# Kernel tuning notes

Measured on AMD Instinct MI355X. Metric: run time of the kernel, lower is better.

## Reference

```python
import jax, jax.numpy as jnp
import numpy as np

N_NODES, N_EDGES, IN_F = 20000, 320000, 64
H1, H2 = 2, 2          # attn heads per GATv2 layer
D1, D2 = 128, 128      # gnn_size per layer
NM = [128, 128]        # nodemlp hidden sizes
EM = [512, 256]        # edgemlp hidden sizes
OUT_F = 1
NEG_SLOPE = 0.2


def _lin_init(key, fan_in, fan_out):
    kw, kb = jax.random.split(key)
    s = 1.0 / np.sqrt(fan_in)
    return (jax.random.uniform(kw, (fan_in, fan_out), jnp.float32, -s, s),
            jax.random.uniform(kb, (fan_out,), jnp.float32, -s, s))


def setup_inputs() -> dict:
    key = jax.random.key(0)
    ks = jax.random.split(key, 16)
    x = jax.random.normal(ks[0], (N_NODES, IN_F), jnp.float32)
    src = jax.random.randint(ks[1], (N_EDGES,), 0, N_NODES, jnp.int32)
    dst = jax.random.randint(ks[2], (N_EDGES,), 0, N_NODES, jnp.int32)
    # NodeMLP
    nw0, nb0 = _lin_init(ks[3], IN_F, NM[0])
    nw1, nb1 = _lin_init(ks[4], NM[0], NM[1])
    # GATv2 layer 1 (in=IN_F -> H1*D1)
    g1ws, g1bs = _lin_init(ks[5], IN_F, H1 * D1)
    g1wd, g1bd = _lin_init(ks[6], IN_F, H1 * D1)
    g1a = jax.random.normal(ks[7], (H1, D1), jnp.float32) * (1.0 / np.sqrt(D1))
    # GATv2 layer 2 (in=H1*D1 -> H2*D2)
    g2ws, g2bs = _lin_init(ks[8], H1 * D1, H2 * D2)
    g2wd, g2bd = _lin_init(ks[9], H1 * D1, H2 * D2)
    g2a = jax.random.normal(ks[10], (H2, D2), jnp.float32) * (1.0 / np.sqrt(D2))
    # EdgeMLP: in = 2*(NM[-1] + H2*D2) = 768
    e_in = 2 * (NM[-1] + H2 * D2)
    ew0, eb0 = _lin_init(ks[11], e_in, EM[0])
    ew1, eb1 = _lin_init(ks[12], EM[0], EM[1])
    ew2, eb2 = _lin_init(ks[13], EM[1], OUT_F)
    return dict(x=x, src=src, dst=dst,
                nw0=nw0, nb0=nb0, nw1=nw1, nb1=nb1,
                g1ws=g1ws, g1bs=g1bs, g1wd=g1wd, g1bd=g1bd, g1a=g1a,
                g2ws=g2ws, g2bs=g2bs, g2wd=g2wd, g2bd=g2bd, g2a=g2a,
                ew0=ew0, eb0=eb0, ew1=ew1, eb1=eb1, ew2=ew2, eb2=eb2)


def _segment_softmax(logits, dst, n):
    # logits: (E, H); softmax over edges sharing the same dst node
    m = jax.ops.segment_max(logits, dst, num_segments=n)
    e = jnp.exp(logits - m[dst])
    s = jax.ops.segment_sum(e, dst, num_segments=n)
    return e / s[dst]


def _gatv2(h, src, dst, ws, bs, wd, bd, attn, heads, dim, n):
    fs = (h @ ws + bs).reshape(n, heads, dim)   # fc_src
    fd = (h @ wd + bd).reshape(n, heads, dim)   # fc_dst
    e = jax.nn.leaky_relu(fs[src] + fd[dst], NEG_SLOPE)      # (E,H,D)
    logits = jnp.einsum('ehd,hd->eh', e, attn)               # (E,H)
    a = _segment_softmax(logits, dst, n)                      # (E,H)
    out = jax.ops.segment_sum(a[..., None] * fs[src], dst, num_segments=n)
    return jax.nn.relu(out).reshape(n, heads * dim)           # flatten heads


def reference(x, src, dst,
              nw0, nb0, nw1, nb1,
              g1ws, g1bs, g1wd, g1bd, g1a,
              g2ws, g2bs, g2wd, g2bd, g2a,
              ew0, eb0, ew1, eb1, ew2, eb2):
    n = x.shape[0]
    # NodeMLP (dropout=0 -> identity)
    h1 = jax.nn.relu(x @ nw0 + nb0)
    h1 = jax.nn.relu(h1 @ nw1 + nb1)
    # GCN: two GATv2Conv layers with relu activation, heads flattened
    h2 = _gatv2(x, src, dst, g1ws, g1bs, g1wd, g1bd, g1a, H1, D1, n)
    h2 = _gatv2(h2, src, dst, g2ws, g2bs, g2wd, g2bd, g2a, H2, D2, n)
    # EdgeMLP: gather src/dst, concat, MLP (relu before every layer but first)
    h = jnp.concatenate([h1[src], h1[dst], h2[src], h2[dst]], axis=1)  # (E,768)
    h = h @ ew0 + eb0
    h = jax.nn.relu(h) @ ew1 + eb1
    h = jax.nn.relu(h) @ ew2 + eb2
    return h  # (E, 1) edge scores
```

## Files before the change

kernel.cpp:

```cpp
#include <hip/hip_runtime.h>
#include <hip/hip_bf16.h>

constexpr int N_NODES = 20000;
constexpr int N_EDGES = 320000;

typedef _Float16 half8 __attribute__((ext_vector_type(8)));
typedef _Float16 half4 __attribute__((ext_vector_type(4)));
typedef float    f32x16 __attribute__((ext_vector_type(16)));

__device__ __forceinline__ float lrelu(float x) { return x > 0.f ? x : 0.2f * x; }

__global__ void scan_all_kernel(const int* __restrict__ counts,
                                int* __restrict__ row_off, int* __restrict__ cursor) {
    __shared__ int ps[1024];
    const int t = threadIdx.x;
    const int base = t * 20;
    int loc[20];
    int sum = 0;
#pragma unroll
    for (int i = 0; i < 20; ++i) {
        const int idx = base + i;
        const int v = (idx < N_NODES) ? counts[idx] : 0;
        loc[i] = sum;
        sum += v;
    }
    ps[t] = sum;
    __syncthreads();
    for (int off = 1; off < 1024; off <<= 1) {
        const int v = (t >= off) ? ps[t - off] : 0;
        __syncthreads();
        ps[t] += v;
        __syncthreads();
    }
    const int ex = ps[t] - sum;
#pragma unroll
    for (int i = 0; i < 20; ++i) {
        const int idx = base + i;
        if (idx < N_NODES) {
            row_off[idx] = ex + loc[i];
            cursor[idx]  = ex + loc[i];
        }
    }
    if (t == 0) row_off[N_NODES] = N_EDGES;
}

__global__ void scatter_kernel(const int* __restrict__ src, const int* __restrict__ dst,
                               int* __restrict__ cursor, int* __restrict__ eidx,
                               int* __restrict__ srcs) {
    int e = blockIdx.x * 256 + threadIdx.x;
    if (e < N_EDGES) {
        int p = atomicAdd(&cursor[dst[e]], 1);
        eidx[p] = e;
        srcs[p] = src[e];
    }
}

template <int K, int M>
__device__ __forceinline__ void pack_one(int idx, const float* __restrict__ W,
                                         int r1, int k1, int r2, int joff, int ldw,
                                         _Float16* __restrict__ H) {
    const int l  = idx & 63;
    const int t  = (idx >> 6) % (M / 32);
    const int s  = (idx >> 6) / (M / 32);
    const int j  = joff + t * 32 + (l & 31);
    const int kb = s * 16 + (l >> 5) * 8;
    half8 vh;
#pragma unroll
    for (int i = 0; i < 8; ++i) {
        const int k    = kb + i;
        const int rrow = (k < k1) ? (r1 + k) : (r2 + (k - k1));
        vh[i] = (_Float16)W[(size_t)rrow * ldw + j];
    }
    reinterpret_cast<half8*>(H)[idx] = vh;
}

constexpr int OFF_W1  = 0;
constexpr int OFF_G2S = 16384;
constexpr int OFF_G2D = 24576;
constexpr int OFF_SW0 = 32768;
constexpr int OFF_SW1 = 45056;
constexpr int OFF_DW0 = 57344;
constexpr int OFF_DW1 = 69632;
constexpr int OFF_N1  = 81920;
constexpr int OFF_X   = 83968;
constexpr int PACK_TOT = 89088;
constexpr int PACK_BLK = (PACK_TOT + 255) / 256;
constexpr int HIST_BLK = 1250;

struct PackIn {
    const float *ew1, *g1ws, *g1wd, *g2ws, *g2wd, *ew0, *nw0, *nw1;
    _Float16 *H;
    const int* dst;
    int* counts;
};

__global__ void hist_prepack_kernel(PackIn a) {
    if (blockIdx.x < HIST_BLK) {
        const int e = blockIdx.x * 256 + threadIdx.x;
        if (e < N_EDGES) atomicAdd(&a.counts[a.dst[e]], 1);
        return;
    }
    const int idx = (blockIdx.x - HIST_BLK) * 256 + threadIdx.x;
    if (idx >= PACK_TOT) return;
    _Float16* H = a.H;
    if (idx < OFF_G2S)
        pack_one<512, 256>(idx - OFF_W1, a.ew1, 0, 512, 0, 0, 256, H + OFF_W1 * 8);
    else if (idx < OFF_G2D)
        pack_one<256, 256>(idx - OFF_G2S, a.g2ws, 0, 256, 0, 0, 256, H + OFF_G2S * 8);
    else if (idx < OFF_SW0)
        pack_one<256, 256>(idx - OFF_G2D, a.g2wd, 0, 256, 0, 0, 256, H + OFF_G2D * 8);
    else if (idx < OFF_SW1)
        pack_one<384, 256>(idx - OFF_SW0, a.ew0, 0, 128, 256, 0, 512, H + OFF_SW0 * 8);
    else if (idx < OFF_DW0)
        pack_one<384, 256>(idx - OFF_SW1, a.ew0, 0, 128, 256, 256, 512, H + OFF_SW1 * 8);
    else if (idx < OFF_DW1)
        pack_one<384, 256>(idx - OFF_DW0, a.ew0, 128, 128, 512, 0, 512, H + OFF_DW0 * 8);
    else if (idx < OFF_N1)
        pack_one<384, 256>(idx - OFF_DW1, a.ew0, 128, 128, 512, 256, 512, H + OFF_DW1 * 8);
    else if (idx < OFF_X)
        pack_one<128, 128>(idx - OFF_N1, a.nw1, 0, 128, 0, 0, 128, H + OFF_N1 * 8);
    else {
        const int xi  = idx - OFF_X;
        const int seg = xi >> 10, r = xi & 1023;
        const int sb  = OFF_X + seg * 1024;
        if (seg == 0)
            pack_one<64, 128>(r, a.nw0, 0, 64, 0, 0, 128, H + sb * 8);
        else if (seg <= 2)
            pack_one<64, 128>(r, a.g1ws, 0, 64, 0, (seg - 1) * 128, 256, H + sb * 8);
        else
            pack_one<64, 128>(r, a.g1wd, 0, 64, 0, (seg - 3) * 128, 256, H + sb * 8);
    }
}

struct LinOut { float* y[6]; const float* b[6]; _Float16* yh[6]; int ldy[6]; int relu[6]; };

template <int K, int TJ, int WR, int K1, int LD1, int LD2, int MINW, int SEG>
__global__ __launch_bounds__(256, MINW) void mfma_linear2_kernel(
    const float* __restrict__ X1, const float* __restrict__ X2,
    const _Float16* __restrict__ BHp,
    LinOut lo, int N) {
    constexpr int WC    = 4 / WR;
    constexpr int TILES = WC * TJ;
    const int jb  = blockIdx.y;
    const int tid = threadIdx.x;
    const int wv  = tid >> 6, l = tid & 63;
    const int rg  = (WR == 1) ? 0 : ((WR == 4) ? wv : (wv & 1));
    const int cg  = (WR == 1) ? wv : ((WR == 4) ? 0 : (wv >> 1));
    const int m   = l & 31, h = l >> 5;
    const int row = blockIdx.x * (32 * WR) + rg * 32 + m;
    const int ar  = (row < N) ? row : (N - 1);
    const float* __restrict__ xr1 = X1 + (size_t)ar * LD1;
    const float* __restrict__ xr2 = X2 + (size_t)ar * LD2;
    const half8* __restrict__ BH = reinterpret_cast<const half8*>(BHp) + (size_t)jb * SEG;
    const float* __restrict__ bp = lo.b[jb];
    float* __restrict__ Y = lo.y[jb];
    _Float16* __restrict__ Yh = lo.yh[jb];
    const int ldy = lo.ldy[jb];
    const int rel = lo.relu[jb];

    f32x16 acc[TJ];
#pragma unroll
    for (int jt = 0; jt < TJ; ++jt) {
        const float bv = bp ? bp[cg * TJ * 32 + jt * 32 + m] : 0.f;
#pragma unroll
        for (int r = 0; r < 16; ++r) acc[jt][r] = bv;
    }

    const int kf = h * 8;
    const float* pf = (kf < K1) ? (xr1 + kf) : (xr2 + (kf - K1));
    float4 xa = *reinterpret_cast<const float4*>(pf);
    float4 xb = *reinterpret_cast<const float4*>(pf + 4);

    for (int s = 0; s < K / 16; ++s) {
        const float xs[8] = {xa.x, xa.y, xa.z, xa.w, xb.x, xb.y, xb.z, xb.w};
        if (s + 1 < K / 16) {
            const int kn = (s + 1) * 16 + h * 8;
            const float* pn = (kn < K1) ? (xr1 + kn) : (xr2 + (kn - K1));
            xa = *reinterpret_cast<const float4*>(pn);
            xb = *reinterpret_cast<const float4*>(pn + 4);
        }
        half8 ah, al;
#pragma unroll
        for (int i = 0; i < 8; ++i) {
            const _Float16 hi = (_Float16)xs[i];
            ah[i] = hi;
            al[i] = (_Float16)(xs[i] - (float)hi);
        }
#pragma unroll
        for (int jt = 0; jt < TJ; ++jt) {
            const int fi = (s * TILES + cg * TJ + jt) * 64 + l;
            const half8 bh = BH[fi];
            acc[jt] = __builtin_amdgcn_mfma_f32_32x32x16_f16(ah, bh, acc[jt], 0, 0, 0);
            acc[jt] = __builtin_amdgcn_mfma_f32_32x32x16_f16(al, bh, acc[jt], 0, 0, 0);
        }
    }

    const int rbase = blockIdx.x * (32 * WR) + rg * 32;
#pragma unroll
    for (int jt = 0; jt < TJ; ++jt) {
        const int j = cg * TJ * 32 + jt * 32 + m;
#pragma unroll
        for (int r = 0; r < 16; ++r) {
            const int orow = rbase + (r & 3) + 8 * (r >> 2) + 4 * h;
            if (orow < N) {
                float v = acc[jt][r];
                if (rel) v = fmaxf(v, 0.f);
                if (Y)  Y[(size_t)orow * ldy + j] = v;
                if (Yh) Yh[(size_t)orow * ldy + j] = (_Float16)v;
            }
        }
    }
}

__global__ void gat_fused_kernel(const _Float16* __restrict__ fsh,
                                 const float* __restrict__ fd,
                                 const float* __restrict__ attn,
                                 const int* __restrict__ row_off,
                                 const int* __restrict__ srcs,
                                 float* __restrict__ outp) {
    const int wv = threadIdx.x >> 6, l = threadIdx.x & 63;
    const int n = blockIdx.x * 4 + wv;
    if (n >= N_NODES) return;
    const int base = (l >> 5) * 128 + (l & 31) * 4;
    const float4 fdv = *reinterpret_cast<const float4*>(&fd[n * 256 + base]);
    const float4 av  = *reinterpret_cast<const float4*>(&attn[base]);
    const int s0 = row_off[n], s1 = row_off[n + 1];

    auto LD = [&](int k) {
        return *reinterpret_cast<const half4*>(&fsh[(size_t)srcs[k] * 256 + base]);
    };
    auto LOGIT = [&](const float4& v) {
        float p = lrelu(v.x + fdv.x) * av.x;
        p = fmaf(lrelu(v.y + fdv.y), av.y, p);
        p = fmaf(lrelu(v.z + fdv.z), av.z, p);
        p = fmaf(lrelu(v.w + fdv.w), av.w, p);
        return p;
    };

    float lsum = 0.f;
    float4 acc = {0.f, 0.f, 0.f, 0.f};
    half4 c0 = {0, 0, 0, 0}, c1 = {0, 0, 0, 0}, n0 = {0, 0, 0, 0}, n1 = {0, 0, 0, 0};
    int i = s0;
    if (i     < s1) c0 = LD(i);
    if (i + 1 < s1) c1 = LD(i + 1);
    if (i + 2 < s1) n0 = LD(i + 2);
    if (i + 3 < s1) n1 = LD(i + 3);
    for (; i + 1 < s1; i += 2) {
        const float4 v0 = {(float)c0.x, (float)c0.y, (float)c0.z, (float)c0.w};
        const float4 v1 = {(float)c1.x, (float)c1.y, (float)c1.z, (float)c1.w};
        c0 = n0; c1 = n1;
        if (i + 4 < s1) n0 = LD(i + 4);
        if (i + 5 < s1) n1 = LD(i + 5);
        float p0 = LOGIT(v0);
        float p1 = LOGIT(v1);
#pragma unroll
        for (int off = 1; off < 32; off <<= 1) {
            p0 += __shfl_xor(p0, off);
            p1 += __shfl_xor(p1, off);
        }
        const float w0 = __expf(p0), w1 = __expf(p1);
        lsum += w0 + w1;
        acc.x = fmaf(w1, v1.x, fmaf(w0, v0.x, acc.x));
        acc.y = fmaf(w1, v1.y, fmaf(w0, v0.y, acc.y));
        acc.z = fmaf(w1, v1.z, fmaf(w0, v0.z, acc.z));
        acc.w = fmaf(w1, v1.w, fmaf(w0, v0.w, acc.w));
    }
    if (i < s1) {
        const float4 v0 = {(float)c0.x, (float)c0.y, (float)c0.z, (float)c0.w};
        float p0 = LOGIT(v0);
#pragma unroll
        for (int off = 1; off < 32; off <<= 1) p0 += __shfl_xor(p0, off);
        const float w0 = __expf(p0);
        lsum += w0;
        acc.x = fmaf(w0, v0.x, acc.x);
        acc.y = fmaf(w0, v0.y, acc.y);
        acc.z = fmaf(w0, v0.z, acc.z);
        acc.w = fmaf(w0, v0.w, acc.w);
    }
    const float inv = (s1 > s0) ? 1.f / lsum : 0.f;
    float4 o;
    o.x = fmaxf(acc.x * inv, 0.f);
    o.y = fmaxf(acc.y * inv, 0.f);
    o.z = fmaxf(acc.z * inv, 0.f);
    o.w = fmaxf(acc.w * inv, 0.f);
    *reinterpret_cast<float4*>(&outp[n * 256 + base]) = o;
}

__global__ __launch_bounds__(256, 2) void edge_mlp7_kernel(
    const _Float16* __restrict__ S, const _Float16* __restrict__ Dn,
    const int* __restrict__ srcs, const int* __restrict__ eidx,
    const int* __restrict__ dstf,
    const _Float16* __restrict__ WpH,
    const float* __restrict__ b1, const float* __restrict__ w2,
    const float* __restrict__ b2, float* __restrict__ out) {
    __shared__ __align__(16) _Float16 Bs[2][8][512];
    const int tid = threadIdx.x;
    const int wv  = tid >> 6, l = tid & 63;
    const int m   = l & 31, h = l >> 5;
    const int e0  = blockIdx.x * 128;
    const int slot = e0 + wv * 32 + m;
    const _Float16* __restrict__ Srow = S  + (size_t)srcs[slot] * 512;
    const _Float16* __restrict__ Drow = Dn + (size_t)dstf[eidx[slot]] * 512;

    f32x16 acc[8];
#pragma unroll
    for (int jt = 0; jt < 8; ++jt) {
        const float bv = b1[jt * 32 + m];
#pragma unroll
        for (int r = 0; r < 16; ++r) acc[jt][r] = bv;
    }

#pragma unroll
    for (int c = 0; c < 2; ++c) {
        const int jt = wv * 2 + c;
        *reinterpret_cast<float4*>(&Bs[0][jt][l * 8]) =
            *reinterpret_cast<const float4*>(WpH + ((size_t)jt * 64 + l) * 8);
    }
    half8 sv = *reinterpret_cast<const half8*>(Srow + h * 8);
    half8 dv = *reinterpret_cast<const half8*>(Drow + h * 8);
    __syncthreads();

    for (int s = 0; s < 32; ++s) {
        const int buf = s & 1;
        float4 bst[2];
        if (s < 31) {
#pragma unroll
            for (int c = 0; c < 2; ++c) {
                const int jt = wv * 2 + c;
                bst[c] = *reinterpret_cast<const float4*>(
                    WpH + ((size_t)((s + 1) * 8 + jt) * 64 + l) * 8);
            }
        }
        half8 xh;
#pragma unroll
        for (int i = 0; i < 8; ++i) {
            const _Float16 t = sv[i] + dv[i];
            xh[i] = t > (_Float16)0.f ? t : (_Float16)0.f;
        }
        if (s < 31) {
            const int ko = (s + 1) * 16 + h * 8;
            sv = *reinterpret_cast<const half8*>(Srow + ko);
            dv = *reinterpret_cast<const half8*>(Drow + ko);
        }
#pragma unroll
        for (int jt = 0; jt < 8; ++jt) {
            const half8 bh = *reinterpret_cast<const half8*>(&Bs[buf][jt][l * 8]);
            acc[jt] = __builtin_amdgcn_mfma_f32_32x32x16_f16(xh, bh, acc[jt], 0, 0, 0);
        }
        if (s < 31) {
#pragma unroll
            for (int c = 0; c < 2; ++c) {
                const int jt = wv * 2 + c;
                *reinterpret_cast<float4*>(&Bs[buf ^ 1][jt][l * 8]) = bst[c];
            }
        }
        __syncthreads();
    }

    float part[16];
#pragma unroll
    for (int r = 0; r < 16; ++r) part[r] = 0.f;
#pragma unroll
    for (int jt = 0; jt < 8; ++jt) {
        const float w2v = w2[jt * 32 + m];
#pragma unroll
        for (int r = 0; r < 16; ++r)
            part[r] = fmaf(fmaxf(acc[jt][r], 0.f), w2v, part[r]);
    }
#pragma unroll
    for (int off = 1; off < 32; off <<= 1)
#pragma unroll
        for (int r = 0; r < 16; ++r) part[r] += __shfl_xor(part[r], off);
    if (m == 0) {
        const float b2v = b2[0];
#pragma unroll
        for (int r = 0; r < 16; ++r) {
            const int row = (r & 3) + 8 * (r >> 2) + 4 * h;
            out[eidx[e0 + wv * 32 + row]] = part[r] + b2v;
        }
    }
}

extern "C" void kernel_launch(void* const* d_in, const int* in_sizes, int n_in,
                              void* d_out, int out_size, void* d_ws, size_t ws_size,
                              hipStream_t stream) {
    (void)in_sizes; (void)n_in; (void)out_size; (void)ws_size;
    const float* x    = (const float*)d_in[0];
    const int*   src  = (const int*)d_in[1];
    const int*   dst  = (const int*)d_in[2];
    const float* nw0  = (const float*)d_in[3];
    const float* nb0  = (const float*)d_in[4];
    const float* nw1  = (const float*)d_in[5];
    const float* nb1  = (const float*)d_in[6];
    const float* g1ws = (const float*)d_in[7];
    const float* g1bs = (const float*)d_in[8];
    const float* g1wd = (const float*)d_in[9];
    const float* g1bd = (const float*)d_in[10];
    const float* g1a  = (const float*)d_in[11];
    const float* g2ws = (const float*)d_in[12];
    const float* g2bs = (const float*)d_in[13];
    const float* g2wd = (const float*)d_in[14];
    const float* g2bd = (const float*)d_in[15];
    const float* g2a  = (const float*)d_in[16];
    const float* ew0  = (const float*)d_in[17];
    const float* eb0  = (const float*)d_in[18];
    const float* ew1  = (const float*)d_in[19];
    const float* eb1  = (const float*)d_in[20];
    const float* ew2  = (const float*)d_in[21];
    const float* eb2  = (const float*)d_in[22];
    float* out = (float*)d_out;

    float* wsF = (float*)d_ws;
    float* h1  = wsF;
    float* g2o = wsF + 2560000;
    float* fsb = wsF + 7680000;
    float* fdb = wsF + 12800000;
    float* g1o = wsF + 17920000;
    _Float16* Sh = (_Float16*)(wsF + 7680000);
    _Float16* Dh = (_Float16*)(wsF + 12800000);
    _Float16* fsh = (_Float16*)(wsF + 23040000);
    int* wsI     = (int*)(wsF + 28160000);
    int* row_off = wsI;
    int* cursor  = wsI + 20016;
    int* eidx    = wsI + 40032;
    int* srcs    = wsI + 360032;
    _Float16* pkH = (_Float16*)((char*)d_ws + 115361280);

    hipMemsetAsync(cursor, 0, N_NODES * sizeof(int), stream);
    PackIn pin{ew1, g1ws, g1wd, g2ws, g2wd, ew0, nw0, nw1, pkH, dst, cursor};
    hist_prepack_kernel<<<HIST_BLK + PACK_BLK, 256, 0, stream>>>(pin);
    scan_all_kernel<<<1, 1024, 0, stream>>>(cursor, row_off, cursor);
    scatter_kernel<<<1250, 256, 0, stream>>>(src, dst, cursor, eidx, srcs);

    {   LinOut lo{};
        lo.y[0] = fsb;        lo.b[0] = nb0;        lo.ldy[0] = 128; lo.relu[0] = 1;
        lo.yh[1] = fsh;       lo.b[1] = g1bs;       lo.ldy[1] = 256;
        lo.yh[2] = fsh + 128; lo.b[2] = g1bs + 128; lo.ldy[2] = 256;
        lo.y[3] = fdb;        lo.b[3] = g1bd;       lo.ldy[3] = 256;
        lo.y[4] = fdb + 128;  lo.b[4] = g1bd + 128; lo.ldy[4] = 256;
        mfma_linear2_kernel<64, 1, 1, 64, 64, 64, 4, 1024>
            <<<dim3(625, 5), 256, 0, stream>>>(x, x, pkH + OFF_X * 8, lo, N_NODES); }

    {   LinOut lo{};
        lo.y[0] = h1; lo.b[0] = nb1; lo.ldy[0] = 128; lo.relu[0] = 1;
        mfma_linear2_kernel<128, 1, 1, 128, 128, 128, 4, 0>
            <<<dim3(625, 1), 256, 0, stream>>>(fsb, fsb, pkH + OFF_N1 * 8, lo, N_NODES); }

    gat_fused_kernel<<<5000, 256, 0, stream>>>(fsh, fdb, g1a, row_off, srcs, g1o);

    {   LinOut lo{};
        lo.yh[0] = fsh; lo.b[0] = g2bs; lo.ldy[0] = 256;
        lo.y[1] = fdb;  lo.b[1] = g2bd; lo.ldy[1] = 256;
        mfma_linear2_kernel<256, 8, 4, 256, 256, 256, 2, 8192>
            <<<dim3(157, 2), 256, 0, stream>>>(g1o, g1o, pkH + OFF_G2S * 8, lo, N_NODES); }
    gat_fused_kernel<<<5000, 256, 0, stream>>>(fsh, fdb, g2a, row_off, srcs, g2o);

    {   LinOut lo{};
        lo.yh[0] = Sh;       lo.ldy[0] = 512;
        lo.yh[1] = Sh + 256; lo.ldy[1] = 512;
        lo.yh[2] = Dh;       lo.b[2] = eb0;       lo.ldy[2] = 512;
        lo.yh[3] = Dh + 256; lo.b[3] = eb0 + 256; lo.ldy[3] = 512;
        mfma_linear2_kernel<384, 8, 4, 128, 128, 256, 2, 12288>
            <<<dim3(157, 4), 256, 0, stream>>>(h1, g2o, pkH + OFF_SW0 * 8, lo, N_NODES); }

    edge_mlp7_kernel<<<N_EDGES / 128, 256, 0, stream>>>(Sh, Dh, srcs, eidx, dst,
                                                        pkH + OFF_W1 * 8,
                                                        eb1, ew2, eb2, out);
}
```

Baseline: 514.7 us.

## Merge independent kernels, unroll GAT gather by four, split edge MLP across eight waves

The edge scatter now shares one launch with the first node linear layer, and the first GAT aggregation shares one launch with the second NodeMLP layer. Each pair is independent work split by block index, so two launches go away and the pairs can overlap. The GAT gather loop now handles four edges per iteration with deeper prefetch, which adds memory-level parallelism at the cost of more registers. The edge MLP now uses 512-thread blocks that split the 256 output columns across two wave groups and combine partial sums in shared memory, which lowers accumulator register pressure per wave but adds a block barrier and a shared-memory reduction.

Result: slower. 559.0 us (+8.6%).

```diff
diff --git a/kernel.cpp b/kernel.cpp
--- a/kernel.cpp
+++ b/kernel.cpp
@@ -42,17 +42,6 @@
         }
     }
     if (t == 0) row_off[N_NODES] = N_EDGES;
-}
-
-__global__ void scatter_kernel(const int* __restrict__ src, const int* __restrict__ dst,
-                               int* __restrict__ cursor, int* __restrict__ eidx,
-                               int* __restrict__ srcs) {
-    int e = blockIdx.x * 256 + threadIdx.x;
-    if (e < N_EDGES) {
-        int p = atomicAdd(&cursor[dst[e]], 1);
-        eidx[p] = e;
-        srcs[p] = src[e];
-    }
 }
 
 template <int K, int M>
@@ -134,20 +123,19 @@
 
 struct LinOut { float* y[6]; const float* b[6]; _Float16* yh[6]; int ldy[6]; int relu[6]; };
 
-template <int K, int TJ, int WR, int K1, int LD1, int LD2, int MINW, int SEG>
-__global__ __launch_bounds__(256, MINW) void mfma_linear2_kernel(
+template <int K, int TJ, int WR, int K1, int LD1, int LD2, int SEG>
+__device__ __forceinline__ void linear_body(
+    int bx, int jb,
     const float* __restrict__ X1, const float* __restrict__ X2,
-    const _Float16* __restrict__ BHp,
-    LinOut lo, int N) {
+    const _Float16* __restrict__ BHp, const LinOut& lo, int N) {
     constexpr int WC    = 4 / WR;
     constexpr int TILES = WC * TJ;
-    const int jb  = blockIdx.y;
     const int tid = threadIdx.x;
     const int wv  = tid >> 6, l = tid & 63;
     const int rg  = (WR == 1) ? 0 : ((WR == 4) ? wv : (wv & 1));
     const int cg  = (WR == 1) ? wv : ((WR == 4) ? 0 : (wv >> 1));
     const int m   = l & 31, h = l >> 5;
-    const int row = blockIdx.x * (32 * WR) + rg * 32 + m;
+    const int row = bx * (32 * WR) + rg * 32 + m;
     const int ar  = (row < N) ? row : (N - 1);
     const float* __restrict__ xr1 = X1 + (size_t)ar * LD1;
     const float* __restrict__ xr2 = X2 + (size_t)ar * LD2;
@@ -195,7 +183,7 @@
         }
     }
 
-    const int rbase = blockIdx.x * (32 * WR) + rg * 32;
+    const int rbase = bx * (32 * WR) + rg * 32;
 #pragma unroll
     for (int jt = 0; jt < TJ; ++jt) {
         const int j = cg * TJ * 32 + jt * 32 + m;
@@ -212,15 +200,20 @@
     }
 }
 
-__global__ void gat_fused_kernel(const _Float16* __restrict__ fsh,
-                                 const float* __restrict__ fd,
-                                 const float* __restrict__ attn,
-                                 const int* __restrict__ row_off,
-                                 const int* __restrict__ srcs,
-                                 float* __restrict__ outp) {
-    const int wv = threadIdx.x >> 6, l = threadIdx.x & 63;
-    const int n = blockIdx.x * 4 + wv;
-    if (n >= N_NODES) return;
+template <int K, int TJ, int WR, int K1, int LD1, int LD2, int MINW, int SEG>
+__global__ __launch_bounds__(256, MINW) void mfma_linear2_kernel(
+    const float* __restrict__ X1, const float* __restrict__ X2,
+    const _Float16* __restrict__ BHp, LinOut lo, int N) {
+    linear_body<K, TJ, WR, K1, LD1, LD2, SEG>(blockIdx.x, blockIdx.y, X1, X2, BHp, lo, N);
+}
+
+__device__ __forceinline__ void gat_body(int n, const _Float16* __restrict__ fsh,
+                                         const float* __restrict__ fd,
+                                         const float* __restrict__ attn,
+                                         const int* __restrict__ row_off,
+                                         const int* __restrict__ srcs,
+                                         float* __restrict__ outp) {
+    const int l = threadIdx.x & 63;
     const int base = (l >> 5) * 128 + (l & 31) * 4;
     const float4 fdv = *reinterpret_cast<const float4*>(&fd[n * 256 + base]);
     const float4 av  = *reinterpret_cast<const float4*>(&attn[base]);
@@ -239,43 +232,55 @@
 
     float lsum = 0.f;
     float4 acc = {0.f, 0.f, 0.f, 0.f};
-    half4 c0 = {0, 0, 0, 0}, c1 = {0, 0, 0, 0}, n0 = {0, 0, 0, 0}, n1 = {0, 0, 0, 0};
+    half4 c[4], nx[4];
+#pragma unroll
+    for (int k = 0; k < 4; ++k) { c[k] = half4{0, 0, 0, 0}; nx[k] = half4{0, 0, 0, 0}; }
     int i = s0;
-    if (i     < s1) c0 = LD(i);
-    if (i + 1 < s1) c1 = LD(i + 1);
-    if (i + 2 < s1) n0 = LD(i + 2);
-    if (i + 3 < s1) n1 = LD(i + 3);
-    for (; i + 1 < s1; i += 2) {
-        const float4 v0 = {(float)c0.x, (float)c0.y, (float)c0.z, (float)c0.w};
-        const float4 v1 = {(float)c1.x, (float)c1.y, (float)c1.z, (float)c1.w};
-        c0 = n0; c1 = n1;
-        if (i + 4 < s1) n0 = LD(i + 4);
-        if (i + 5 < s1) n1 = LD(i + 5);
-        float p0 = LOGIT(v0);
-        float p1 = LOGIT(v1);
-#pragma unroll
-        for (int off = 1; off < 32; off <<= 1) {
-            p0 += __shfl_xor(p0, off);
-            p1 += __shfl_xor(p1, off);
-        }
-        const float w0 = __expf(p0), w1 = __expf(p1);
-        lsum += w0 + w1;
-        acc.x = fmaf(w1, v1.x, fmaf(w0, v0.x, acc.x));
-        acc.y = fmaf(w1, v1.y, fmaf(w0, v0.y, acc.y));
-        acc.z = fmaf(w1, v1.z, fmaf(w0, v0.z, acc.z));
-        acc.w = fmaf(w1, v1.w, fmaf(w0, v0.w, acc.w));
-    }
-    if (i < s1) {
-        const float4 v0 = {(float)c0.x, (float)c0.y, (float)c0.z, (float)c0.w};
-        float p0 = LOGIT(v0);
-#pragma unroll
-        for (int off = 1; off < 32; off <<= 1) p0 += __shfl_xor(p0, off);
-        const float w0 = __expf(p0);
-        lsum += w0;
-        acc.x = fmaf(w0, v0.x, acc.x);
-        acc.y = fmaf(w0, v0.y, acc.y);
-        acc.z = fmaf(w0, v0.z, acc.z);
-        acc.w = fmaf(w0, v0.w, acc.w);
+#pragma unroll
+    for (int k = 0; k < 4; ++k) if (i + k < s1) c[k] = LD(i + k);
+#pragma unroll
+    for (int k = 0; k < 4; ++k) if (i + 4 + k < s1) nx[k] = LD(i + 4 + k);
+
+    for (; i + 3 < s1; i += 4) {
+        float4 v[4];
+#pragma unroll
+        for (int k = 0; k < 4; ++k)
+            v[k] = float4{(float)c[k].x, (float)c[k].y, (float)c[k].z, (float)c[k].w};
+#pragma unroll
+        for (int k = 0; k < 4; ++k) {
+            c[k] = nx[k];
+            if (i + 8 + k < s1) nx[k] = LD(i + 8 + k);
+        }
+        float p[4];
+#pragma unroll
+        for (int k = 0; k < 4; ++k) p[k] = LOGIT(v[k]);
+#pragma unroll
+        for (int off = 1; off < 32; off <<= 1)
+#pragma unroll
+            for (int k = 0; k < 4; ++k) p[k] += __shfl_xor(p[k], off);
+        float w[4];
+#pragma unroll
+        for (int k = 0; k < 4; ++k) w[k] = __expf(p[k]);
+        lsum += (w[0] + w[1]) + (w[2] + w[3]);
+#pragma unroll
+        for (int k = 0; k < 4; ++k) {
+            acc.x = fmaf(w[k], v[k].x, acc.x);
+            acc.y = fmaf(w[k], v[k].y, acc.y);
+            acc.z = fmaf(w[k], v[k].z, acc.z);
+            acc.w = fmaf(w[k], v[k].w, acc.w);
+        }
+    }
+    for (int k = 0; i < s1; ++i, ++k) {
+        const float4 v = {(float)c[k].x, (float)c[k].y, (float)c[k].z, (float)c[k].w};
+        float p = LOGIT(v);
+#pragma unroll
+        for (int off = 1; off < 32; off <<= 1) p += __shfl_xor(p, off);
+        const float w = __expf(p);
+        lsum += w;
+        acc.x = fmaf(w, v.x, acc.x);
+        acc.y = fmaf(w, v.y, acc.y);
+        acc.z = fmaf(w, v.z, acc.z);
+        acc.w = fmaf(w, v.w, acc.w);
     }
     const float inv = (s1 > s0) ? 1.f / lsum : 0.f;
     float4 o;
@@ -286,7 +291,46 @@
     *reinterpret_cast<float4*>(&outp[n * 256 + base]) = o;
 }
 
-__global__ __launch_bounds__(256, 2) void edge_mlp7_kernel(
+__global__ __launch_bounds__(256, 4) void gat_fused_kernel(
+    const _Float16* __restrict__ fsh, const float* __restrict__ fd,
+    const float* __restrict__ attn, const int* __restrict__ row_off,
+    const int* __restrict__ srcs, float* __restrict__ outp) {
+    const int n = blockIdx.x * 4 + (threadIdx.x >> 6);
+    if (n < N_NODES) gat_body(n, fsh, fd, attn, row_off, srcs, outp);
+}
+
+__global__ __launch_bounds__(256, 4) void scatter_xfc_kernel(
+    const int* __restrict__ src, const int* __restrict__ dst,
+    int* __restrict__ cursor, int* __restrict__ eidx, int* __restrict__ srcs,
+    const float* __restrict__ x, const _Float16* __restrict__ BH, LinOut lo) {
+    if (blockIdx.x < 1250) {
+        const int e = blockIdx.x * 256 + threadIdx.x;
+        if (e < N_EDGES) {
+            const int p = atomicAdd(&cursor[dst[e]], 1);
+            eidx[p] = e;
+            srcs[p] = src[e];
+        }
+        return;
+    }
+    const int bx = blockIdx.x - 1250;
+    linear_body<64, 1, 1, 64, 64, 64, 1024>(bx % 625, bx / 625, x, x, BH, lo, N_NODES);
+}
+
+__global__ __launch_bounds__(256, 4) void gat1_fc2_kernel(
+    const _Float16* __restrict__ fsh, const float* __restrict__ fd,
+    const float* __restrict__ attn, const int* __restrict__ row_off,
+    const int* __restrict__ srcs, float* __restrict__ outp,
+    const float* __restrict__ fsb, const _Float16* __restrict__ BHn1, LinOut lo2) {
+    if (blockIdx.x < 5000) {
+        const int n = blockIdx.x * 4 + (threadIdx.x >> 6);
+        if (n < N_NODES) gat_body(n, fsh, fd, attn, row_off, srcs, outp);
+        return;
+    }
+    linear_body<128, 1, 1, 128, 128, 128, 0>(blockIdx.x - 5000, 0, fsb, fsb, BHn1,
+                                             lo2, N_NODES);
+}
+
+__global__ __launch_bounds__(512, 4) void edge_mlp9_kernel(
     const _Float16* __restrict__ S, const _Float16* __restrict__ Dn,
     const int* __restrict__ srcs, const int* __restrict__ eidx,
     const int* __restrict__ dstf,
@@ -294,43 +338,36 @@
     const float* __restrict__ b1, const float* __restrict__ w2,
     const float* __restrict__ b2, float* __restrict__ out) {
     __shared__ __align__(16) _Float16 Bs[2][8][512];
+    __shared__ float q[2][128];
     const int tid = threadIdx.x;
     const int wv  = tid >> 6, l = tid & 63;
+    const int eg  = wv & 3, jg = wv >> 2;
     const int m   = l & 31, h = l >> 5;
     const int e0  = blockIdx.x * 128;
-    const int slot = e0 + wv * 32 + m;
+    const int slot = e0 + eg * 32 + m;
     const _Float16* __restrict__ Srow = S  + (size_t)srcs[slot] * 512;
     const _Float16* __restrict__ Drow = Dn + (size_t)dstf[eidx[slot]] * 512;
 
-    f32x16 acc[8];
-#pragma unroll
-    for (int jt = 0; jt < 8; ++jt) {
-        const float bv = b1[jt * 32 + m];
+    f32x16 acc[4];
+#pragma unroll
+    for (int jt = 0; jt < 4; ++jt) {
+        const float bv = b1[jg * 128 + jt * 32 + m];
 #pragma unroll
         for (int r = 0; r < 16; ++r) acc[jt][r] = bv;
     }
 
-#pragma unroll
-    for (int c = 0; c < 2; ++c) {
-        const int jt = wv * 2 + c;
-        *reinterpret_cast<float4*>(&Bs[0][jt][l * 8]) =
-            *reinterpret_cast<const float4*>(WpH + ((size_t)jt * 64 + l) * 8);
-    }
+    *reinterpret_cast<float4*>(&Bs[0][wv][l * 8]) =
+        *reinterpret_cast<const float4*>(WpH + ((size_t)wv * 64 + l) * 8);
     half8 sv = *reinterpret_cast<const half8*>(Srow + h * 8);
     half8 dv = *reinterpret_cast<const half8*>(Drow + h * 8);
     __syncthreads();
 
     for (int s = 0; s < 32; ++s) {
         const int buf = s & 1;
-        float4 bst[2];
-        if (s < 31) {
-#pragma unroll
-            for (int c = 0; c < 2; ++c) {
-                const int jt = wv * 2 + c;
-                bst[c] = *reinterpret_cast<const float4*>(
-                    WpH + ((size_t)((s + 1) * 8 + jt) * 64 + l) * 8);
-            }
-        }
+        float4 bst;
+        if (s < 31)
+            bst = *reinterpret_cast<const float4*>(
+                WpH + ((size_t)((s + 1) * 8 + wv) * 64 + l) * 8);
         half8 xh;
 #pragma unroll
         for (int i = 0; i < 8; ++i) {
@@ -343,17 +380,12 @@
             dv = *reinterpret_cast<const half8*>(Drow + ko);
         }
 #pragma unroll
-        for (int jt = 0; jt < 8; ++jt) {
-            const half8 bh = *reinterpret_cast<const half8*>(&Bs[buf][jt][l * 8]);
+        for (int jt = 0; jt < 4; ++jt) {
+            const half8 bh = *reinterpret_cast<const half8*>(&Bs[buf][jg * 4 + jt][l * 8]);
             acc[jt] = __builtin_amdgcn_mfma_f32_32x32x16_f16(xh, bh, acc[jt], 0, 0, 0);
         }
-        if (s < 31) {
-#pragma unroll
-            for (int c = 0; c < 2; ++c) {
-                const int jt = wv * 2 + c;
-                *reinterpret_cast<float4*>(&Bs[buf ^ 1][jt][l * 8]) = bst[c];
-            }
-        }
+        if (s < 31)
+            *reinterpret_cast<float4*>(&Bs[buf ^ 1][wv][l * 8]) = bst;
         __syncthreads();
     }
 
@@ -361,8 +393,8 @@
 #pragma unroll
     for (int r = 0; r < 16; ++r) part[r] = 0.f;
 #pragma unroll
-    for (int jt = 0; jt < 8; ++jt) {
-        const float w2v = w2[jt * 32 + m];
+    for (int jt = 0; jt < 4; ++jt) {
+        const float w2v = w2[jg * 128 + jt * 32 + m];
 #pragma unroll
         for (int r = 0; r < 16; ++r)
             part[r] = fmaf(fmaxf(acc[jt][r], 0.f), w2v, part[r]);
@@ -372,13 +404,14 @@
 #pragma unroll
         for (int r = 0; r < 16; ++r) part[r] += __shfl_xor(part[r], off);
     if (m == 0) {
-        const float b2v = b2[0];
 #pragma unroll
         for (int r = 0; r < 16; ++r) {
             const int row = (r & 3) + 8 * (r >> 2) + 4 * h;
-            out[eidx[e0 + wv * 32 + row]] = part[r] + b2v;
-        }
-    }
+            q[jg][eg * 32 + row] = part[r];
+        }
+    }
+    __syncthreads();
+    if (tid < 128) out[eidx[e0 + tid]] = q[0][tid] + q[1][tid] + b2[0];
 }
 
 extern "C" void kernel_launch(void* const* d_in, const int* in_sizes, int n_in,
@@ -430,7 +463,6 @@
     PackIn pin{ew1, g1ws, g1wd, g2ws, g2wd, ew0, nw0, nw1, pkH, dst, cursor};
     hist_prepack_kernel<<<HIST_BLK + PACK_BLK, 256, 0, stream>>>(pin);
     scan_all_kernel<<<1, 1024, 0, stream>>>(cursor, row_off, cursor);
-    scatter_kernel<<<1250, 256, 0, stream>>>(src, dst, cursor, eidx, srcs);
 
     {   LinOut lo{};
         lo.y[0] = fsb;        lo.b[0] = nb0;        lo.ldy[0] = 128; lo.relu[0] = 1;
@@ -438,15 +470,13 @@
         lo.yh[2] = fsh + 128; lo.b[2] = g1bs + 128; lo.ldy[2] = 256;
         lo.y[3] = fdb;        lo.b[3] = g1bd;       lo.ldy[3] = 256;
         lo.y[4] = fdb + 128;  lo.b[4] = g1bd + 128; lo.ldy[4] = 256;
-        mfma_linear2_kernel<64, 1, 1, 64, 64, 64, 4, 1024>
-            <<<dim3(625, 5), 256, 0, stream>>>(x, x, pkH + OFF_X * 8, lo, N_NODES); }
-
-    {   LinOut lo{};
-        lo.y[0] = h1; lo.b[0] = nb1; lo.ldy[0] = 128; lo.relu[0] = 1;
-        mfma_linear2_kernel<128, 1, 1, 128, 128, 128, 4, 0>
-            <<<dim3(625, 1), 256, 0, stream>>>(fsb, fsb, pkH + OFF_N1 * 8, lo, N_NODES); }
-
-    gat_fused_kernel<<<5000, 256, 0, stream>>>(fsh, fdb, g1a, row_off, srcs, g1o);
+        scatter_xfc_kernel<<<1250 + 3125, 256, 0, stream>>>(
+            src, dst, cursor, eidx, srcs, x, pkH + OFF_X * 8, lo); }
+
+    {   LinOut lo2{};
+        lo2.y[0] = h1; lo2.b[0] = nb1; lo2.ldy[0] = 128; lo2.relu[0] = 1;
+        gat1_fc2_kernel<<<5000 + 625, 256, 0, stream>>>(
+            fsh, fdb, g1a, row_off, srcs, g1o, fsb, pkH + OFF_N1 * 8, lo2); }
 
     {   LinOut lo{};
         lo.yh[0] = fsh; lo.b[0] = g2bs; lo.ldy[0] = 256;
@@ -463,7 +493,7 @@
         mfma_linear2_kernel<384, 8, 4, 128, 128, 256, 2, 12288>
             <<<dim3(157, 4), 256, 0, stream>>>(h1, g2o, pkH + OFF_SW0 * 8, lo, N_NODES); }
 
-    edge_mlp7_kernel<<<N_EDGES / 128, 256, 0, stream>>>(Sh, Dh, srcs, eidx, dst,
+    edge_mlp9_kernel<<<N_EDGES / 128, 512, 0, stream>>>(Sh, Dh, srcs, eidx, dst,
                                                         pkH + OFF_W1 * 8,
                                                         eb1, ew2, eb2, out);
 }
```
